# Kernel tuning notes

Measured on AMD Instinct MI355X. Metric: run time of the kernel, lower is better.

The kernel has to match this reference:

```python
import jax, jax.numpy as jnp
import numpy as np

R = 2          # candidate_radius
TEMP = 0.1     # temperature
MIN_E = 3
MAX_E = 8      # max_edges_per_node
EPS = 1e-6


def _neighbors(H, W, r):
    # grid neighbor indices (N,K) and relative positions (K,2), clamped at borders
    ys, xs = np.meshgrid(np.arange(H), np.arange(W), indexing='ij')
    idx_grid = ys * W + xs
    nbrs, rel = [], []
    for dy in range(-r, r + 1):
        for dx in range(-r, r + 1):
            if dy == 0 and dx == 0:
                continue
            ny = np.clip(ys + dy, 0, H - 1)
            nx = np.clip(xs + dx, 0, W - 1)
            nbrs.append(idx_grid[ny, nx].ravel())
            rel.append([dx / r, dy / r])
    return jnp.asarray(np.stack(nbrs, 1)), jnp.asarray(np.array(rel, np.float32))


def setup_inputs() -> dict:
    key = jax.random.key(0)
    ks = jax.random.split(key, 12)
    B, C, H, W = 2, 64, 128, 128
    hid = 64
    ein = 2 * C + 2  # edge scorer input dim
    s = 0.05
    return {
        'x':  jax.random.normal(ks[0], (B, C, H, W), jnp.float32),
        'W1': jax.random.normal(ks[1], (hid, ein), jnp.float32) * s,
        'b1': jnp.zeros((hid,), jnp.float32),
        'W2': jax.random.normal(ks[2], (hid // 2, hid), jnp.float32) * s,
        'b2': jnp.zeros((hid // 2,), jnp.float32),
        'W3': jax.random.normal(ks[3], (1, hid // 2), jnp.float32) * s,
        'b3': jnp.zeros((1,), jnp.float32),
        'thr': jnp.asarray(0.0, jnp.float32),
        'Wm': jax.random.normal(ks[4], (C, C), jnp.float32) * s,
        'bm': jnp.zeros((C,), jnp.float32),
        'Wo': jax.random.normal(ks[5], (C, C), jnp.float32) * s,
        'bo': jnp.zeros((C,), jnp.float32),
    }


def reference(x, W1, b1, W2, b2, W3, b3, thr, Wm, bm, Wo, bo):
    B, C, H, W = x.shape
    N = H * W
    nbr, rel = _neighbors(H, W, R)          # (N,K), (K,2)
    K = nbr.shape[1]

    nodes = x.transpose(0, 2, 3, 1).reshape(B, N, C)   # (B,N,C)
    h_tgt = jnp.take(nodes, nbr, axis=1)               # (B,N,K,C) gather neighbors

    # edge scorer layer1: split W1 over [h_src | h_tgt | rel_pos] to avoid (B,N,K,2C+2) concat
    z_src = nodes @ W1[:, :C].T                        # (B,N,hid)
    z_tgt = h_tgt @ W1[:, C:2 * C].T                   # (B,N,K,hid)
    z_pos = rel @ W1[:, 2 * C:].T                      # (K,hid)
    h1 = jax.nn.relu(z_src[:, :, None, :] + z_tgt + z_pos[None, None] + b1)
    h2 = jax.nn.relu(h1 @ W2.T + b2)
    edge_scores = jax.nn.sigmoid((h2 @ W3.T + b3)[..., 0])   # (B,N,K)

    thr_v = jax.nn.sigmoid(thr)
    keep_prob = jax.nn.sigmoid((edge_scores - thr_v) / TEMP)
    mask_thr = edge_scores >= thr_v
    counts = mask_thr.sum(axis=2)                       # (B,N)

    def topk_mask(k):
        _, idx = jax.lax.top_k(edge_scores, k)          # (B,N,k)
        return jax.nn.one_hot(idx, K, dtype=jnp.float32).sum(-2) > 0

    m_max = topk_mask(min(MAX_E, K))
    m_min = topk_mask(min(MIN_E, K))
    use_max = (counts > MAX_E)[..., None]
    use_min = (counts < MIN_E)[..., None]
    use_t = ~use_max & ~use_min
    final_mask = (use_max & m_max) | (use_min & m_min) | (use_t & mask_thr)

    msgs = jax.nn.relu(h_tgt @ Wm.T + bm)               # (B,N,K,C)
    w = (edge_scores * keep_prob * final_mask.astype(edge_scores.dtype))[..., None]
    agg = (msgs * w).sum(axis=2) / (w.sum(axis=2) + EPS)  # (B,N,C)

    out = nodes + agg @ Wo.T + bo
    return out.reshape(B, H, W, C).transpose(0, 3, 1, 2)
```

## Files before the change

kernel.cpp:

```cpp
#include <hip/hip_runtime.h>
#include <hip/hip_bf16.h>
#include <math.h>

#define NNODES 16384
#define KE 24

typedef float f32x4 __attribute__((ext_vector_type(4)));
typedef short bf16x8 __attribute__((ext_vector_type(8)));
typedef unsigned u32x4 __attribute__((ext_vector_type(4)));

union fragcast { u32x4 u; bf16x8 b; };

static __device__ __forceinline__ void split3(float v, unsigned& uh,
                                              unsigned& ul, unsigned& um) {
    union { float f; unsigned u; } a; a.f = v;
    uh = a.u & 0xFFFF0000u;
    union { unsigned u; float f; } h; h.u = uh;
    float r1 = v - h.f;
    union { float f; unsigned u; } b; b.f = r1;
    ul = b.u & 0xFFFF0000u;
    union { unsigned u; float f; } l; l.u = ul;
    float r2 = r1 - l.f;
    union { float f; unsigned u; } c; c.f = r2;
    um = c.u;
}

static __device__ __forceinline__ unsigned pack_hi16(unsigned even, unsigned odd) {
    return __builtin_amdgcn_perm(odd, even, 0x07060302u);
}

__global__ __launch_bounds__(256) void precompute_k(
    const float* __restrict__ x, const float* __restrict__ W1,
    const float* __restrict__ Wm, const float* __restrict__ b1,
    const float* __restrict__ bm,
    float* __restrict__ zsrc, float* __restrict__ ztgt, float* __restrict__ msg,
    float* __restrict__ zpos)
{
    __shared__ float xt[64][128];
    __shared__ float wl[64][64];
    const int t = threadIdx.x;
    const int mat = blockIdx.x >> 8;
    const int tile = blockIdx.x & 255;
    const int n0 = tile * 128;
    const int b = n0 >> 14;
    const int nl0 = n0 & (NNODES - 1);
    const float* xb = x + (size_t)b * 64 * NNODES + nl0;

    if (blockIdx.x == 0) {
        for (int idx = t; idx < KE * 64; idx += 256) {
            int k = idx >> 6, h = idx & 63;
            int kk = k + (k >= 12 ? 1 : 0);
            int q5 = (kk * 52) >> 8;
            int dy = q5 - 2, dx = kk - 5 * q5 - 2;
            zpos[idx] = W1[h * 130 + 128] * (dx * 0.5f)
                      + W1[h * 130 + 129] * (dy * 0.5f);
        }
    }

    #pragma unroll
    for (int r = 0; r < 8; ++r) {
        int idx = r * 256 + t;
        int c = idx >> 5, j4 = idx & 31;
        float4 v = *(const float4*)(xb + (size_t)c * NNODES + j4 * 4);
        *(float4*)&xt[c][j4 * 4] = v;
    }
    #pragma unroll
    for (int r = 0; r < 16; ++r) {
        int idx = r * 256 + t;
        int c = idx >> 6, h = idx & 63;
        float v = (mat == 0) ? W1[h * 130 + c]
                : (mat == 1) ? W1[h * 130 + 64 + c]
                             : Wm[h * 64 + c];
        (&wl[0][0])[idx] = v;
    }
    __syncthreads();

    const int i = t >> 5;
    const int j = t & 31;

    float acc[8][4];
    #pragma unroll
    for (int a = 0; a < 8; ++a)
        #pragma unroll
        for (int bb = 0; bb < 4; ++bb) acc[a][bb] = 0.f;

    #pragma unroll 4
    for (int c = 0; c < 64; ++c) {
        float4 w0 = *(const float4*)&wl[c][i * 8];
        float4 w1 = *(const float4*)&wl[c][i * 8 + 4];
        float4 x0 = *(const float4*)&xt[c][j * 4];
        float wv[8] = {w0.x, w0.y, w0.z, w0.w, w1.x, w1.y, w1.z, w1.w};
        float xv[4] = {x0.x, x0.y, x0.z, x0.w};
        #pragma unroll
        for (int a = 0; a < 8; ++a)
            #pragma unroll
            for (int bb = 0; bb < 4; ++bb)
                acc[a][bb] = fmaf(wv[a], xv[bb], acc[a][bb]);
    }

    #pragma unroll
    for (int a = 0; a < 8; ++a) {
        float bv = (mat == 0) ? b1[i * 8 + a] : (mat == 2) ? bm[i * 8 + a] : 0.f;
        #pragma unroll
        for (int bb = 0; bb < 4; ++bb) {
            float v = acc[a][bb] + bv;
            acc[a][bb] = (mat == 2) ? fmaxf(v, 0.f) : v;
        }
    }

    float* dst = (mat == 0) ? zsrc : (mat == 1) ? ztgt : msg;
    #pragma unroll
    for (int bb = 0; bb < 4; ++bb) {
        float* o = dst + (size_t)(n0 + j * 4 + bb) * 64 + i * 8;
        *(float4*)o       = make_float4(acc[0][bb], acc[1][bb], acc[2][bb], acc[3][bb]);
        *(float4*)(o + 4) = make_float4(acc[4][bb], acc[5][bb], acc[6][bb], acc[7][bb]);
    }
}

__global__ __launch_bounds__(256, 3) void score_k(
    const float* __restrict__ zsrc, const float* __restrict__ ztgt,
    const float* __restrict__ zpos, const float* __restrict__ W2,
    const float* __restrict__ b2, const float* __restrict__ W3,
    const float* __restrict__ b3, float* __restrict__ scores)
{
    __shared__ fragcast fraglds[64 * 13];
    __shared__ float zpl[24 * 68];

    const int t = threadIdx.x;
    const int l = t & 63;
    const int lcol = l & 15;
    const int lgrp = l >> 4;
    const int w = t >> 6;
    const int wave = blockIdx.x * 4 + w;

    #pragma unroll
    for (int r = 0; r < 6; ++r) {
        int idx = r * 256 + t;
        zpl[(idx >> 6) * 68 + (idx & 63)] = zpos[idx];
    }
    {
        const int jt = w >> 1, kt = w & 1;
        fragcast fh, fl, fl2;
        const float* wr = W2 + (size_t)(jt * 16 + lcol) * 64 + kt * 32 + lgrp * 8;
        #pragma unroll
        for (int d = 0; d < 4; ++d) {
            unsigned h0, l0, m0, h1, l1, m1;
            split3(wr[2 * d],     h0, l0, m0);
            split3(wr[2 * d + 1], h1, l1, m1);
            fh.u[d]  = pack_hi16(h0, h1);
            fl.u[d]  = pack_hi16(l0, l1);
            fl2.u[d] = pack_hi16(m0, m1);
        }
        fraglds[l * 13 + 0 + jt * 2 + kt] = fh;
        fraglds[l * 13 + 4 + jt * 2 + kt] = fl;
        fraglds[l * 13 + 8 + jt * 2 + kt] = fl2;
    }
    __syncthreads();

    const fragcast* fb = &fraglds[l * 13];
    const f32x4 b2l0 = *(const f32x4*)(b2 + lgrp * 4);
    const f32x4 b2l1 = *(const f32x4*)(b2 + 16 + lgrp * 4);
    const f32x4 w3l0 = *(const f32x4*)(W3 + lgrp * 4);
    const f32x4 w3l1 = *(const f32x4*)(W3 + 16 + lgrp * 4);
    const float b3s = b3[0];

    const int node0 = wave * 2;

    #pragma unroll
    for (int Mt = 0; Mt < 3; ++Mt) {
        const int ke = Mt * 16 + lcol;
        const int nsel = (ke >= 24) ? 1 : 0;
        const int node = node0 + nsel;
        const int k = ke - 24 * nsel;
        const int bb = node >> 14;
        const int nl = node & (NNODES - 1);
        const int yy = nl >> 7, xx = nl & 127;
        const int kk = k + (k >= 12 ? 1 : 0);
        const int q5 = (kk * 52) >> 8;
        const int dy = q5 - 2, dx = kk - 5 * q5 - 2;
        const int ny = min(max(yy + dy, 0), 127);
        const int nx = min(max(xx + dx, 0), 127);
        const int nbn = (bb << 14) + (ny << 7) + nx;

        const float* zs = zsrc + (size_t)node * 64 + lgrp * 8;
        const float* zt = ztgt + (size_t)nbn * 64 + lgrp * 8;
        const float* zp = &zpl[k * 68 + lgrp * 8];

        f32x4 ac0A = {0.f,0.f,0.f,0.f}, ac0B = {0.f,0.f,0.f,0.f};
        f32x4 ac1A = {0.f,0.f,0.f,0.f}, ac1B = {0.f,0.f,0.f,0.f};

        #pragma unroll
        for (int kt = 0; kt < 2; ++kt) {
            const int o = kt * 32;
            float4 a0 = *(const float4*)(zs + o);
            float4 a1 = *(const float4*)(zs + o + 4);
            float4 t0 = *(const float4*)(zt + o);
            float4 t1 = *(const float4*)(zt + o + 4);
            float4 p0 = *(const float4*)(zp + o);
            float4 p1 = *(const float4*)(zp + o + 4);
            float v[8];
            v[0] = fmaxf(a0.x + t0.x + p0.x, 0.f);
            v[1] = fmaxf(a0.y + t0.y + p0.y, 0.f);
            v[2] = fmaxf(a0.z + t0.z + p0.z, 0.f);
            v[3] = fmaxf(a0.w + t0.w + p0.w, 0.f);
            v[4] = fmaxf(a1.x + t1.x + p1.x, 0.f);
            v[5] = fmaxf(a1.y + t1.y + p1.y, 0.f);
            v[6] = fmaxf(a1.z + t1.z + p1.z, 0.f);
            v[7] = fmaxf(a1.w + t1.w + p1.w, 0.f);

            fragcast Bh, Bl, Bl2;
            #pragma unroll
            for (int d = 0; d < 4; ++d) {
                unsigned h0, l0, m0, h1, l1, m1;
                split3(v[2 * d],     h0, l0, m0);
                split3(v[2 * d + 1], h1, l1, m1);
                Bh.u[d]  = pack_hi16(h0, h1);
                Bl.u[d]  = pack_hi16(l0, l1);
                Bl2.u[d] = pack_hi16(m0, m1);
            }

            ac0A = __builtin_amdgcn_mfma_f32_16x16x32_bf16(fb[0 + kt].b,  Bh.b,  ac0A, 0, 0, 0);
            ac1A = __builtin_amdgcn_mfma_f32_16x16x32_bf16(fb[2 + kt].b,  Bh.b,  ac1A, 0, 0, 0);
            ac0B = __builtin_amdgcn_mfma_f32_16x16x32_bf16(fb[4 + kt].b,  Bh.b,  ac0B, 0, 0, 0);
            ac1B = __builtin_amdgcn_mfma_f32_16x16x32_bf16(fb[6 + kt].b,  Bh.b,  ac1B, 0, 0, 0);
            ac0A = __builtin_amdgcn_mfma_f32_16x16x32_bf16(fb[8 + kt].b,  Bh.b,  ac0A, 0, 0, 0);
            ac1A = __builtin_amdgcn_mfma_f32_16x16x32_bf16(fb[10 + kt].b, Bh.b,  ac1A, 0, 0, 0);
            ac0B = __builtin_amdgcn_mfma_f32_16x16x32_bf16(fb[0 + kt].b,  Bl.b,  ac0B, 0, 0, 0);
            ac1B = __builtin_amdgcn_mfma_f32_16x16x32_bf16(fb[2 + kt].b,  Bl.b,  ac1B, 0, 0, 0);
            ac0A = __builtin_amdgcn_mfma_f32_16x16x32_bf16(fb[4 + kt].b,  Bl.b,  ac0A, 0, 0, 0);
            ac1A = __builtin_amdgcn_mfma_f32_16x16x32_bf16(fb[6 + kt].b,  Bl.b,  ac1A, 0, 0, 0);
            ac0B = __builtin_amdgcn_mfma_f32_16x16x32_bf16(fb[0 + kt].b,  Bl2.b, ac0B, 0, 0, 0);
            ac1B = __builtin_amdgcn_mfma_f32_16x16x32_bf16(fb[2 + kt].b,  Bl2.b, ac1B, 0, 0, 0);
        }

        const f32x4 s0 = ac0A + ac0B;
        const f32x4 s1 = ac1A + ac1B;
        float sacc = 0.f;
        #pragma unroll
        for (int q = 0; q < 4; ++q) {
            sacc = fmaf(fmaxf(s0[q] + b2l0[q], 0.f), w3l0[q], sacc);
            sacc = fmaf(fmaxf(s1[q] + b2l1[q], 0.f), w3l1[q], sacc);
        }
        sacc += __shfl_xor(sacc, 16);
        sacc += __shfl_xor(sacc, 32);
        float sig = 1.f / (1.f + expf(-(sacc + b3s)));
        if (l < 16)
            scores[(size_t)node0 * 24 + Mt * 16 + l] = sig;
    }
}

__global__ __launch_bounds__(256) void agg_k(
    const float* __restrict__ x, const float* __restrict__ scores,
    const float* __restrict__ msg, const float* __restrict__ Wo,
    const float* __restrict__ bo, const float* __restrict__ thrp,
    float* __restrict__ out)
{
    __shared__ float sc[768];
    __shared__ float wl[768];
    __shared__ float sumw[32];
    __shared__ float aggL[32][64];
    __shared__ float ot[64][33];

    const int t = threadIdx.x;
    const int n0 = blockIdx.x * 32;
    const int b = n0 >> 14;
    const int nl0 = n0 & (NNODES - 1);
    const float thr_v = 1.f / (1.f + expf(-thrp[0]));

    #pragma unroll
    for (int rep = 0; rep < 3; ++rep)
        sc[rep * 256 + t] = scores[(size_t)n0 * 24 + rep * 256 + t];
    __syncthreads();

    #pragma unroll
    for (int rep = 0; rep < 3; ++rep) {
        int e = rep * 256 + t;
        int nl = (int)(((unsigned)(e >> 3) * 171u) >> 9);
        int k = e - nl * 24;
        float s_e = sc[e];
        int rank = 0, cnt = 0;
        #pragma unroll
        for (int j = 0; j < 24; ++j) {
            float sj = sc[nl * 24 + j];
            rank += (sj > s_e || (sj == s_e && j < k)) ? 1 : 0;
            cnt  += (sj >= thr_v) ? 1 : 0;
        }
        bool mask = (cnt > 8) ? (rank < 8)
                  : ((cnt < 3) ? (rank < 3) : (s_e >= thr_v));
        float keep = 1.f / (1.f + expf(-(s_e - thr_v) * 10.f));
        wl[e] = mask ? s_e * keep : 0.f;
    }
    __syncthreads();

    if (t < 32) {
        float s = 0.f;
        #pragma unroll
        for (int k = 0; k < 24; ++k) s += wl[t * 24 + k];
        sumw[t] = s + 1e-6f;
    }
    __syncthreads();

    const int lane = t & 63;
    const int g4 = t >> 6;

    #pragma unroll
    for (int it = 0; it < 8; ++it) {
        int nl = g4 + it * 4;
        int nn = nl0 + nl;
        int yy = nn >> 7, xx = nn & 127;
        float acc = 0.f;
        #pragma unroll
        for (int k = 0; k < 24; ++k) {
            int kk = k + (k >= 12 ? 1 : 0);
            int q5 = (kk * 52) >> 8;
            int dy = q5 - 2, dx = kk - 5 * q5 - 2;
            int ny = min(max(yy + dy, 0), 127);
            int nx = min(max(xx + dx, 0), 127);
            int nb = (b << 14) + (ny << 7) + nx;
            acc = fmaf(wl[nl * 24 + k], msg[(size_t)nb * 64 + lane], acc);
        }
        aggL[nl][lane] = acc / sumw[nl];
    }

    float4 wo[16];
    #pragma unroll
    for (int c4 = 0; c4 < 16; ++c4) wo[c4] = ((const float4*)Wo)[lane * 16 + c4];
    __syncthreads();

    #pragma unroll
    for (int it = 0; it < 8; ++it) {
        int nl = g4 + it * 4;
        const float4* ar = (const float4*)aggL[nl];
        float a0 = 0.f, a1 = 0.f, a2 = 0.f, a3 = 0.f;
        #pragma unroll
        for (int c4 = 0; c4 < 16; ++c4) {
            float4 wv = wo[c4];
            float4 av = ar[c4];
            a0 = fmaf(av.x, wv.x, a0);
            a1 = fmaf(av.y, wv.y, a1);
            a2 = fmaf(av.z, wv.z, a2);
            a3 = fmaf(av.w, wv.w, a3);
        }
        float v = (a0 + a1) + (a2 + a3) + bo[lane]
                + x[(size_t)b * 64 * NNODES + (size_t)lane * NNODES + nl0 + nl];
        ot[lane][nl] = v;
    }
    __syncthreads();

    #pragma unroll
    for (int rep = 0; rep < 2; ++rep) {
        int idx = rep * 256 + t;
        int o = idx >> 3, p = idx & 7;
        float4 v = make_float4(ot[o][4 * p + 0], ot[o][4 * p + 1],
                               ot[o][4 * p + 2], ot[o][4 * p + 3]);
        *(float4*)(out + (size_t)b * 64 * NNODES + (size_t)o * NNODES + nl0 + 4 * p) = v;
    }
}

extern "C" void kernel_launch(void* const* d_in, const int* in_sizes, int n_in,
                              void* d_out, int out_size, void* d_ws, size_t ws_size,
                              hipStream_t stream)
{
    const float* x   = (const float*)d_in[0];
    const float* W1  = (const float*)d_in[1];
    const float* b1  = (const float*)d_in[2];
    const float* W2  = (const float*)d_in[3];
    const float* b2  = (const float*)d_in[4];
    const float* W3  = (const float*)d_in[5];
    const float* b3  = (const float*)d_in[6];
    const float* thr = (const float*)d_in[7];
    const float* Wm  = (const float*)d_in[8];
    const float* bm  = (const float*)d_in[9];
    const float* Wo  = (const float*)d_in[10];
    const float* bo  = (const float*)d_in[11];
    float* out = (float*)d_out;
    float* ws  = (float*)d_ws;

    float* zsrc   = ws;
    float* ztgt   = ws + 2097152;
    float* msg    = ws + 4194304;
    float* scores = ws + 6291456;
    float* zpos   = ws + 7077888;

    hipLaunchKernelGGL(precompute_k, dim3(768), dim3(256), 0, stream,
                       x, W1, Wm, b1, bm, zsrc, ztgt, msg, zpos);
    hipLaunchKernelGGL(score_k, dim3(4096), dim3(256), 0, stream,
                       zsrc, ztgt, zpos, W2, b2, W3, b3, scores);
    hipLaunchKernelGGL(agg_k, dim3(1024), dim3(256), 0, stream,
                       x, scores, msg, Wo, bo, thr, out);
}
```

Before: 89.41 us.

## Stage neighbor z_tgt halo tile in LDS for score kernel

```diff
diff --git a/kernel.cpp b/kernel.cpp
--- a/kernel.cpp
+++ b/kernel.cpp
@@ -117,7 +117,7 @@
     }
 }
 
-__global__ __launch_bounds__(256, 3) void score_k(
+__global__ __launch_bounds__(256, 4) void score_k(
     const float* __restrict__ zsrc, const float* __restrict__ ztgt,
     const float* __restrict__ zpos, const float* __restrict__ W2,
     const float* __restrict__ b2, const float* __restrict__ W3,
@@ -125,18 +125,32 @@
 {
     __shared__ fragcast fraglds[64 * 13];
     __shared__ float zpl[24 * 68];
+    __shared__ float ztile[100 * 68];
 
     const int t = threadIdx.x;
     const int l = t & 63;
     const int lcol = l & 15;
     const int lgrp = l >> 4;
     const int w = t >> 6;
-    const int wave = blockIdx.x * 4 + w;
+    const int blkbase = blockIdx.x * 16;
+    const int b = blkbase >> 14;
+    const int y = (blkbase >> 7) & 127;
+    const int x0 = blkbase & 127;
 
     #pragma unroll
     for (int r = 0; r < 6; ++r) {
         int idx = r * 256 + t;
         zpl[(idx >> 6) * 68 + (idx & 63)] = zpos[idx];
+    }
+    for (int i = t; i < 1600; i += 256) {
+        int row = i >> 4, f4 = i & 15;
+        int wy = (row * 3277) >> 16;
+        int cx = row - wy * 20;
+        int gy = min(max(y + wy - 2, 0), 127);
+        int gx = min(max(x0 + cx - 2, 0), 127);
+        int gn = (b << 14) + (gy << 7) + gx;
+        *(float4*)&ztile[row * 68 + f4 * 4] =
+            *(const float4*)(ztgt + (size_t)gn * 64 + f4 * 4);
     }
     {
         const int jt = w >> 1, kt = w & 1;
@@ -164,88 +178,87 @@
     const f32x4 w3l1 = *(const f32x4*)(W3 + 16 + lgrp * 4);
     const float b3s = b3[0];
 
-    const int node0 = wave * 2;
-
-    #pragma unroll
-    for (int Mt = 0; Mt < 3; ++Mt) {
-        const int ke = Mt * 16 + lcol;
-        const int nsel = (ke >= 24) ? 1 : 0;
-        const int node = node0 + nsel;
-        const int k = ke - 24 * nsel;
-        const int bb = node >> 14;
-        const int nl = node & (NNODES - 1);
-        const int yy = nl >> 7, xx = nl & 127;
-        const int kk = k + (k >= 12 ? 1 : 0);
-        const int q5 = (kk * 52) >> 8;
-        const int dy = q5 - 2, dx = kk - 5 * q5 - 2;
-        const int ny = min(max(yy + dy, 0), 127);
-        const int nx = min(max(xx + dx, 0), 127);
-        const int nbn = (bb << 14) + (ny << 7) + nx;
-
-        const float* zs = zsrc + (size_t)node * 64 + lgrp * 8;
-        const float* zt = ztgt + (size_t)nbn * 64 + lgrp * 8;
-        const float* zp = &zpl[k * 68 + lgrp * 8];
-
-        f32x4 ac0A = {0.f,0.f,0.f,0.f}, ac0B = {0.f,0.f,0.f,0.f};
-        f32x4 ac1A = {0.f,0.f,0.f,0.f}, ac1B = {0.f,0.f,0.f,0.f};
-
-        #pragma unroll
-        for (int kt = 0; kt < 2; ++kt) {
-            const int o = kt * 32;
-            float4 a0 = *(const float4*)(zs + o);
-            float4 a1 = *(const float4*)(zs + o + 4);
-            float4 t0 = *(const float4*)(zt + o);
-            float4 t1 = *(const float4*)(zt + o + 4);
-            float4 p0 = *(const float4*)(zp + o);
-            float4 p1 = *(const float4*)(zp + o + 4);
-            float v[8];
-            v[0] = fmaxf(a0.x + t0.x + p0.x, 0.f);
-            v[1] = fmaxf(a0.y + t0.y + p0.y, 0.f);
-            v[2] = fmaxf(a0.z + t0.z + p0.z, 0.f);
-            v[3] = fmaxf(a0.w + t0.w + p0.w, 0.f);
-            v[4] = fmaxf(a1.x + t1.x + p1.x, 0.f);
-            v[5] = fmaxf(a1.y + t1.y + p1.y, 0.f);
-            v[6] = fmaxf(a1.z + t1.z + p1.z, 0.f);
-            v[7] = fmaxf(a1.w + t1.w + p1.w, 0.f);
-
-            fragcast Bh, Bl, Bl2;
+    #pragma unroll 1
+    for (int p = 0; p < 2; ++p) {
+        const int node0 = blkbase + w * 4 + p * 2;
+
+        #pragma unroll
+        for (int Mt = 0; Mt < 3; ++Mt) {
+            const int ke = Mt * 16 + lcol;
+            const int nsel = (ke >= 24) ? 1 : 0;
+            const int node = node0 + nsel;
+            const int k = ke - 24 * nsel;
+            const int xloc = (node & 127) - x0;
+            const int kk = k + (k >= 12 ? 1 : 0);
+            const int q5 = (kk * 52) >> 8;
+            const int dy = q5 - 2, dx = kk - 5 * q5 - 2;
+            const int trow = (dy + 2) * 20 + xloc + dx + 2;
+
+            const float* zs = zsrc + (size_t)node * 64 + lgrp * 8;
+            const float* zt = &ztile[trow * 68 + lgrp * 8];
+            const float* zp = &zpl[k * 68 + lgrp * 8];
+
+            f32x4 ac0A = {0.f,0.f,0.f,0.f}, ac0B = {0.f,0.f,0.f,0.f};
+            f32x4 ac1A = {0.f,0.f,0.f,0.f}, ac1B = {0.f,0.f,0.f,0.f};
+
             #pragma unroll
-            for (int d = 0; d < 4; ++d) {
-                unsigned h0, l0, m0, h1, l1, m1;
-                split3(v[2 * d],     h0, l0, m0);
-                split3(v[2 * d + 1], h1, l1, m1);
-                Bh.u[d]  = pack_hi16(h0, h1);
-                Bl.u[d]  = pack_hi16(l0, l1);
-                Bl2.u[d] = pack_hi16(m0, m1);
+            for (int kt = 0; kt < 2; ++kt) {
+                const int o = kt * 32;
+                float4 a0 = *(const float4*)(zs + o);
+                float4 a1 = *(const float4*)(zs + o + 4);
+                float4 t0 = *(const float4*)(zt + o);
+                float4 t1 = *(const float4*)(zt + o + 4);
+                float4 p0 = *(const float4*)(zp + o);
+                float4 p1 = *(const float4*)(zp + o + 4);
+                float v[8];
+                v[0] = fmaxf(a0.x + t0.x + p0.x, 0.f);
+                v[1] = fmaxf(a0.y + t0.y + p0.y, 0.f);
+                v[2] = fmaxf(a0.z + t0.z + p0.z, 0.f);
+                v[3] = fmaxf(a0.w + t0.w + p0.w, 0.f);
+                v[4] = fmaxf(a1.x + t1.x + p1.x, 0.f);
+                v[5] = fmaxf(a1.y + t1.y + p1.y, 0.f);
+                v[6] = fmaxf(a1.z + t1.z + p1.z, 0.f);
+                v[7] = fmaxf(a1.w + t1.w + p1.w, 0.f);
+
+                fragcast Bh, Bl, Bl2;
+                #pragma unroll
+                for (int d = 0; d < 4; ++d) {
+                    unsigned h0, l0, m0, h1, l1, m1;
+                    split3(v[2 * d],     h0, l0, m0);
+                    split3(v[2 * d + 1], h1, l1, m1);
+                    Bh.u[d]  = pack_hi16(h0, h1);
+                    Bl.u[d]  = pack_hi16(l0, l1);
+                    Bl2.u[d] = pack_hi16(m0, m1);
+                }
+
+                ac0A = __builtin_amdgcn_mfma_f32_16x16x32_bf16(fb[0 + kt].b,  Bh.b,  ac0A, 0, 0, 0);
+                ac1A = __builtin_amdgcn_mfma_f32_16x16x32_bf16(fb[2 + kt].b,  Bh.b,  ac1A, 0, 0, 0);
+                ac0B = __builtin_amdgcn_mfma_f32_16x16x32_bf16(fb[4 + kt].b,  Bh.b,  ac0B, 0, 0, 0);
+                ac1B = __builtin_amdgcn_mfma_f32_16x16x32_bf16(fb[6 + kt].b,  Bh.b,  ac1B, 0, 0, 0);
+                ac0A = __builtin_amdgcn_mfma_f32_16x16x32_bf16(fb[8 + kt].b,  Bh.b,  ac0A, 0, 0, 0);
+                ac1A = __builtin_amdgcn_mfma_f32_16x16x32_bf16(fb[10 + kt].b, Bh.b,  ac1A, 0, 0, 0);
+                ac0B = __builtin_amdgcn_mfma_f32_16x16x32_bf16(fb[0 + kt].b,  Bl.b,  ac0B, 0, 0, 0);
+                ac1B = __builtin_amdgcn_mfma_f32_16x16x32_bf16(fb[2 + kt].b,  Bl.b,  ac1B, 0, 0, 0);
+                ac0A = __builtin_amdgcn_mfma_f32_16x16x32_bf16(fb[4 + kt].b,  Bl.b,  ac0A, 0, 0, 0);
+                ac1A = __builtin_amdgcn_mfma_f32_16x16x32_bf16(fb[6 + kt].b,  Bl.b,  ac1A, 0, 0, 0);
+                ac0B = __builtin_amdgcn_mfma_f32_16x16x32_bf16(fb[0 + kt].b,  Bl2.b, ac0B, 0, 0, 0);
+                ac1B = __builtin_amdgcn_mfma_f32_16x16x32_bf16(fb[2 + kt].b,  Bl2.b, ac1B, 0, 0, 0);
             }
 
-            ac0A = __builtin_amdgcn_mfma_f32_16x16x32_bf16(fb[0 + kt].b,  Bh.b,  ac0A, 0, 0, 0);
-            ac1A = __builtin_amdgcn_mfma_f32_16x16x32_bf16(fb[2 + kt].b,  Bh.b,  ac1A, 0, 0, 0);
-            ac0B = __builtin_amdgcn_mfma_f32_16x16x32_bf16(fb[4 + kt].b,  Bh.b,  ac0B, 0, 0, 0);
-            ac1B = __builtin_amdgcn_mfma_f32_16x16x32_bf16(fb[6 + kt].b,  Bh.b,  ac1B, 0, 0, 0);
-            ac0A = __builtin_amdgcn_mfma_f32_16x16x32_bf16(fb[8 + kt].b,  Bh.b,  ac0A, 0, 0, 0);
-            ac1A = __builtin_amdgcn_mfma_f32_16x16x32_bf16(fb[10 + kt].b, Bh.b,  ac1A, 0, 0, 0);
-            ac0B = __builtin_amdgcn_mfma_f32_16x16x32_bf16(fb[0 + kt].b,  Bl.b,  ac0B, 0, 0, 0);
-            ac1B = __builtin_amdgcn_mfma_f32_16x16x32_bf16(fb[2 + kt].b,  Bl.b,  ac1B, 0, 0, 0);
-            ac0A = __builtin_amdgcn_mfma_f32_16x16x32_bf16(fb[4 + kt].b,  Bl.b,  ac0A, 0, 0, 0);
-            ac1A = __builtin_amdgcn_mfma_f32_16x16x32_bf16(fb[6 + kt].b,  Bl.b,  ac1A, 0, 0, 0);
-            ac0B = __builtin_amdgcn_mfma_f32_16x16x32_bf16(fb[0 + kt].b,  Bl2.b, ac0B, 0, 0, 0);
-            ac1B = __builtin_amdgcn_mfma_f32_16x16x32_bf16(fb[2 + kt].b,  Bl2.b, ac1B, 0, 0, 0);
-        }
-
-        const f32x4 s0 = ac0A + ac0B;
-        const f32x4 s1 = ac1A + ac1B;
-        float sacc = 0.f;
-        #pragma unroll
-        for (int q = 0; q < 4; ++q) {
-            sacc = fmaf(fmaxf(s0[q] + b2l0[q], 0.f), w3l0[q], sacc);
-            sacc = fmaf(fmaxf(s1[q] + b2l1[q], 0.f), w3l1[q], sacc);
-        }
-        sacc += __shfl_xor(sacc, 16);
-        sacc += __shfl_xor(sacc, 32);
-        float sig = 1.f / (1.f + expf(-(sacc + b3s)));
-        if (l < 16)
-            scores[(size_t)node0 * 24 + Mt * 16 + l] = sig;
+            const f32x4 s0 = ac0A + ac0B;
+            const f32x4 s1 = ac1A + ac1B;
+            float sacc = 0.f;
+            #pragma unroll
+            for (int q = 0; q < 4; ++q) {
+                sacc = fmaf(fmaxf(s0[q] + b2l0[q], 0.f), w3l0[q], sacc);
+                sacc = fmaf(fmaxf(s1[q] + b2l1[q], 0.f), w3l1[q], sacc);
+            }
+            sacc += __shfl_xor(sacc, 16);
+            sacc += __shfl_xor(sacc, 32);
+            float sig = 1.f / (1.f + expf(-(sacc + b3s)));
+            if (l < 16)
+                scores[(size_t)node0 * 24 + Mt * 16 + l] = sig;
+        }
     }
 }
 
@@ -384,7 +397,7 @@
 
     hipLaunchKernelGGL(precompute_k, dim3(768), dim3(256), 0, stream,
                        x, W1, Wm, b1, bm, zsrc, ztgt, msg, zpos);
-    hipLaunchKernelGGL(score_k, dim3(4096), dim3(256), 0, stream,
+    hipLaunchKernelGGL(score_k, dim3(2048), dim3(256), 0, stream,
                        zsrc, ztgt, zpos, W2, b2, W3, b3, scores);
     hipLaunchKernelGGL(agg_k, dim3(1024), dim3(256), 0, stream,
                        x, scores, msg, Wo, bo, thr, out);
```

Result: slower. 91.37 us (+2.2%).

## Switch score MLP split-precision MFMA from bf16x3 to scaled fp16x2, pretranspose weights

Applied to the files above, without the earlier changes.

```diff
diff --git a/kernel.cpp b/kernel.cpp
--- a/kernel.cpp
+++ b/kernel.cpp
@@ -6,35 +6,40 @@
 #define KE 24
 
 typedef float f32x4 __attribute__((ext_vector_type(4)));
-typedef short bf16x8 __attribute__((ext_vector_type(8)));
 typedef unsigned u32x4 __attribute__((ext_vector_type(4)));
-
-union fragcast { u32x4 u; bf16x8 b; };
-
-static __device__ __forceinline__ void split3(float v, unsigned& uh,
-                                              unsigned& ul, unsigned& um) {
-    union { float f; unsigned u; } a; a.f = v;
-    uh = a.u & 0xFFFF0000u;
-    union { unsigned u; float f; } h; h.u = uh;
-    float r1 = v - h.f;
-    union { float f; unsigned u; } b; b.f = r1;
-    ul = b.u & 0xFFFF0000u;
-    union { unsigned u; float f; } l; l.u = ul;
-    float r2 = r1 - l.f;
-    union { float f; unsigned u; } c; c.f = r2;
-    um = c.u;
-}
-
-static __device__ __forceinline__ unsigned pack_hi16(unsigned even, unsigned odd) {
-    return __builtin_amdgcn_perm(odd, even, 0x07060302u);
+typedef __fp16 half2_t __attribute__((ext_vector_type(2)));
+typedef _Float16 half8_t __attribute__((ext_vector_type(8)));
+
+union fragcast { u32x4 u; half8_t h; half2_t h2[4]; };
+
+__global__ void aux_k(const float* __restrict__ W1, const float* __restrict__ Wm,
+                      float* __restrict__ zpos, float* __restrict__ wt)
+{
+    int t = threadIdx.x;
+    for (int idx = t; idx < KE * 64; idx += 256) {
+        int k = idx >> 6, h = idx & 63;
+        int kk = k + (k >= 12 ? 1 : 0);
+        int q5 = (kk * 52) >> 8;
+        int dy = q5 - 2;
+        int dx = kk - 5 * q5 - 2;
+        zpos[idx] = W1[h * 130 + 128] * (dx * 0.5f)
+                  + W1[h * 130 + 129] * (dy * 0.5f);
+    }
+    for (int idx = t; idx < 3 * 64 * 64; idx += 256) {
+        int mat = idx >> 12;
+        int r = idx & 4095;
+        int c = r >> 6, h = r & 63;
+        float v = (mat == 0) ? W1[h * 130 + c]
+                : (mat == 1) ? W1[h * 130 + 64 + c]
+                             : Wm[h * 64 + c];
+        wt[idx] = v;
+    }
 }
 
 __global__ __launch_bounds__(256) void precompute_k(
-    const float* __restrict__ x, const float* __restrict__ W1,
-    const float* __restrict__ Wm, const float* __restrict__ b1,
-    const float* __restrict__ bm,
-    float* __restrict__ zsrc, float* __restrict__ ztgt, float* __restrict__ msg,
-    float* __restrict__ zpos)
+    const float* __restrict__ x, const float* __restrict__ wt,
+    const float* __restrict__ b1, const float* __restrict__ bm,
+    float* __restrict__ zsrc, float* __restrict__ ztgt, float* __restrict__ msg)
 {
     __shared__ float xt[64][128];
     __shared__ float wl[64][64];
@@ -46,17 +51,6 @@
     const int nl0 = n0 & (NNODES - 1);
     const float* xb = x + (size_t)b * 64 * NNODES + nl0;
 
-    if (blockIdx.x == 0) {
-        for (int idx = t; idx < KE * 64; idx += 256) {
-            int k = idx >> 6, h = idx & 63;
-            int kk = k + (k >= 12 ? 1 : 0);
-            int q5 = (kk * 52) >> 8;
-            int dy = q5 - 2, dx = kk - 5 * q5 - 2;
-            zpos[idx] = W1[h * 130 + 128] * (dx * 0.5f)
-                      + W1[h * 130 + 129] * (dy * 0.5f);
-        }
-    }
-
     #pragma unroll
     for (int r = 0; r < 8; ++r) {
         int idx = r * 256 + t;
@@ -65,13 +59,9 @@
         *(float4*)&xt[c][j4 * 4] = v;
     }
     #pragma unroll
-    for (int r = 0; r < 16; ++r) {
+    for (int r = 0; r < 4; ++r) {
         int idx = r * 256 + t;
-        int c = idx >> 6, h = idx & 63;
-        float v = (mat == 0) ? W1[h * 130 + c]
-                : (mat == 1) ? W1[h * 130 + 64 + c]
-                             : Wm[h * 64 + c];
-        (&wl[0][0])[idx] = v;
+        ((float4*)&wl[0][0])[idx] = ((const float4*)(wt + mat * 4096))[idx];
     }
     __syncthreads();
 
@@ -140,20 +130,20 @@
     }
     {
         const int jt = w >> 1, kt = w & 1;
-        fragcast fh, fl, fl2;
+        fragcast fh, fl;
         const float* wr = W2 + (size_t)(jt * 16 + lcol) * 64 + kt * 32 + lgrp * 8;
         #pragma unroll
         for (int d = 0; d < 4; ++d) {
-            unsigned h0, l0, m0, h1, l1, m1;
-            split3(wr[2 * d],     h0, l0, m0);
-            split3(wr[2 * d + 1], h1, l1, m1);
-            fh.u[d]  = pack_hi16(h0, h1);
-            fl.u[d]  = pack_hi16(l0, l1);
-            fl2.u[d] = pack_hi16(m0, m1);
+            float e0 = wr[2 * d] * 64.f;
+            float e1 = wr[2 * d + 1] * 64.f;
+            half2_t hh = __builtin_amdgcn_cvt_pkrtz(e0, e1);
+            float r0 = e0 - (float)hh[0];
+            float r1 = e1 - (float)hh[1];
+            fh.h2[d] = hh;
+            fl.h2[d] = __builtin_amdgcn_cvt_pkrtz(r0, r1);
         }
         fraglds[l * 13 + 0 + jt * 2 + kt] = fh;
         fraglds[l * 13 + 4 + jt * 2 + kt] = fl;
-        fraglds[l * 13 + 8 + jt * 2 + kt] = fl2;
     }
     __syncthreads();
 
@@ -208,29 +198,23 @@
             v[6] = fmaxf(a1.z + t1.z + p1.z, 0.f);
             v[7] = fmaxf(a1.w + t1.w + p1.w, 0.f);
 
-            fragcast Bh, Bl, Bl2;
+            fragcast Bh, Bl;
             #pragma unroll
             for (int d = 0; d < 4; ++d) {
-                unsigned h0, l0, m0, h1, l1, m1;
-                split3(v[2 * d],     h0, l0, m0);
-                split3(v[2 * d + 1], h1, l1, m1);
-                Bh.u[d]  = pack_hi16(h0, h1);
-                Bl.u[d]  = pack_hi16(l0, l1);
-                Bl2.u[d] = pack_hi16(m0, m1);
+                float e0 = v[2 * d], e1 = v[2 * d + 1];
+                half2_t hh = __builtin_amdgcn_cvt_pkrtz(e0, e1);
+                float r0 = e0 - (float)hh[0];
+                float r1 = e1 - (float)hh[1];
+                Bh.h2[d] = hh;
+                Bl.h2[d] = __builtin_amdgcn_cvt_pkrtz(r0, r1);
             }
 
-            ac0A = __builtin_amdgcn_mfma_f32_16x16x32_bf16(fb[0 + kt].b,  Bh.b,  ac0A, 0, 0, 0);
-            ac1A = __builtin_amdgcn_mfma_f32_16x16x32_bf16(fb[2 + kt].b,  Bh.b,  ac1A, 0, 0, 0);
-            ac0B = __builtin_amdgcn_mfma_f32_16x16x32_bf16(fb[4 + kt].b,  Bh.b,  ac0B, 0, 0, 0);
-            ac1B = __builtin_amdgcn_mfma_f32_16x16x32_bf16(fb[6 + kt].b,  Bh.b,  ac1B, 0, 0, 0);
-            ac0A = __builtin_amdgcn_mfma_f32_16x16x32_bf16(fb[8 + kt].b,  Bh.b,  ac0A, 0, 0, 0);
-            ac1A = __builtin_amdgcn_mfma_f32_16x16x32_bf16(fb[10 + kt].b, Bh.b,  ac1A, 0, 0, 0);
-            ac0B = __builtin_amdgcn_mfma_f32_16x16x32_bf16(fb[0 + kt].b,  Bl.b,  ac0B, 0, 0, 0);
-            ac1B = __builtin_amdgcn_mfma_f32_16x16x32_bf16(fb[2 + kt].b,  Bl.b,  ac1B, 0, 0, 0);
-            ac0A = __builtin_amdgcn_mfma_f32_16x16x32_bf16(fb[4 + kt].b,  Bl.b,  ac0A, 0, 0, 0);
-            ac1A = __builtin_amdgcn_mfma_f32_16x16x32_bf16(fb[6 + kt].b,  Bl.b,  ac1A, 0, 0, 0);
-            ac0B = __builtin_amdgcn_mfma_f32_16x16x32_bf16(fb[0 + kt].b,  Bl2.b, ac0B, 0, 0, 0);
-            ac1B = __builtin_amdgcn_mfma_f32_16x16x32_bf16(fb[2 + kt].b,  Bl2.b, ac1B, 0, 0, 0);
+            ac0A = __builtin_amdgcn_mfma_f32_16x16x32_f16(fb[0 + kt].h, Bh.h, ac0A, 0, 0, 0);
+            ac1A = __builtin_amdgcn_mfma_f32_16x16x32_f16(fb[2 + kt].h, Bh.h, ac1A, 0, 0, 0);
+            ac0B = __builtin_amdgcn_mfma_f32_16x16x32_f16(fb[4 + kt].h, Bh.h, ac0B, 0, 0, 0);
+            ac1B = __builtin_amdgcn_mfma_f32_16x16x32_f16(fb[6 + kt].h, Bh.h, ac1B, 0, 0, 0);
+            ac0B = __builtin_amdgcn_mfma_f32_16x16x32_f16(fb[0 + kt].h, Bl.h, ac0B, 0, 0, 0);
+            ac1B = __builtin_amdgcn_mfma_f32_16x16x32_f16(fb[2 + kt].h, Bl.h, ac1B, 0, 0, 0);
         }
 
         const f32x4 s0 = ac0A + ac0B;
@@ -238,8 +222,8 @@
         float sacc = 0.f;
         #pragma unroll
         for (int q = 0; q < 4; ++q) {
-            sacc = fmaf(fmaxf(s0[q] + b2l0[q], 0.f), w3l0[q], sacc);
-            sacc = fmaf(fmaxf(s1[q] + b2l1[q], 0.f), w3l1[q], sacc);
+            sacc = fmaf(fmaxf(fmaf(s0[q], 0.015625f, b2l0[q]), 0.f), w3l0[q], sacc);
+            sacc = fmaf(fmaxf(fmaf(s1[q], 0.015625f, b2l1[q]), 0.f), w3l1[q], sacc);
         }
         sacc += __shfl_xor(sacc, 16);
         sacc += __shfl_xor(sacc, 32);
@@ -381,9 +365,11 @@
     float* msg    = ws + 4194304;
     float* scores = ws + 6291456;
     float* zpos   = ws + 7077888;
-
+    float* wt     = ws + 7079424;
+
+    hipLaunchKernelGGL(aux_k, dim3(1), dim3(256), 0, stream, W1, Wm, zpos, wt);
     hipLaunchKernelGGL(precompute_k, dim3(768), dim3(256), 0, stream,
-                       x, W1, Wm, b1, bm, zsrc, ztgt, msg, zpos);
+                       x, wt, b1, bm, zsrc, ztgt, msg);
     hipLaunchKernelGGL(score_k, dim3(4096), dim3(256), 0, stream,
                        zsrc, ztgt, zpos, W2, b2, W3, b3, scores);
     hipLaunchKernelGGL(agg_k, dim3(1024), dim3(256), 0, stream,
```

After: 97.81 us. +9.4%, slower.
